# Kernel optimization log

Measured on AMD Instinct MI355X. Metric: run time of the kernel, lower is better.

Reference implementation:

```python
import jax, jax.numpy as jnp
import numpy as np

N_NODES = 50000
N_EDGES = 640000
HIDDEN = 128
EDGE_DIM = 3


def _glorot(key, shape):
    fan_in, fan_out = shape[0], shape[1]
    lim = (6.0 / (fan_in + fan_out)) ** 0.5
    return jax.random.uniform(key, shape, jnp.float32, -lim, lim)


def setup_inputs() -> dict:
    key = jax.random.key(0)
    ks = jax.random.split(key, 12)
    x = jax.random.normal(ks[0], (N_NODES, HIDDEN), jnp.float32)
    edge_index = jax.random.randint(ks[1], (2, N_EDGES), 0, N_NODES, jnp.int64)
    edge_attr = jax.random.normal(ks[2], (N_EDGES, EDGE_DIM), jnp.float32)
    params = {
        "W_msg1": _glorot(ks[3], (2 * HIDDEN + EDGE_DIM, HIDDEN)),
        "b_msg1": jnp.zeros((HIDDEN,), jnp.float32),
        "W_msg2": _glorot(ks[4], (HIDDEN, HIDDEN)),
        "b_msg2": jnp.zeros((HIDDEN,), jnp.float32),
        "W_gate": _glorot(ks[5], (2 * HIDDEN, HIDDEN)),
        "b_gate": jnp.zeros((HIDDEN,), jnp.float32),
        "W_upd1": _glorot(ks[6], (2 * HIDDEN, HIDDEN)),
        "b_upd1": jnp.zeros((HIDDEN,), jnp.float32),
        "W_upd2": _glorot(ks[7], (HIDDEN, HIDDEN)),
        "b_upd2": jnp.zeros((HIDDEN,), jnp.float32),
        "ln_gamma": jnp.ones((HIDDEN,), jnp.float32),
        "ln_beta": jnp.zeros((HIDDEN,), jnp.float32),
    }
    return dict(x=x, edge_index=edge_index, edge_attr=edge_attr, **params)


def reference(x, edge_index, edge_attr, W_msg1, b_msg1, W_msg2, b_msg2,
              W_gate, b_gate, W_upd1, b_upd1, W_upd2, b_upd2, ln_gamma, ln_beta):
    src, dst = edge_index[0], edge_index[1]
    source = x[src]            # [E, H]
    target = x[dst]            # [E, H]
    msg_in = jnp.concatenate([source, target, edge_attr], axis=-1)  # [E, 2H+edge_dim]
    h = jax.nn.relu(msg_in @ W_msg1 + b_msg1)  # dropout is identity in eval
    messages = h @ W_msg2 + b_msg2             # [E, H]
    aggregated = jax.ops.segment_sum(messages, dst, num_segments=x.shape[0])  # [N, H]
    upd_in = jnp.concatenate([x, aggregated], axis=-1)  # [N, 2H]
    gate = jax.nn.sigmoid(upd_in @ W_gate + b_gate)
    update = jax.nn.relu(upd_in @ W_upd1 + b_upd1) @ W_upd2 + b_upd2
    out = gate * update + (1.0 - gate) * x
    # LayerNorm (eps=1e-5, matching torch default)
    mu = jnp.mean(out, axis=-1, keepdims=True)
    var = jnp.var(out, axis=-1, keepdims=True)
    normed = (out - mu) * jax.lax.rsqrt(var + 1e-5)
    return normed * ln_gamma + ln_beta
```

## Files before the change

kernel.cpp:

```cpp
#include <hip/hip_runtime.h>
#include <hip/hip_bf16.h>

#define HID 128

typedef __attribute__((ext_vector_type(8))) short short8;
typedef __attribute__((ext_vector_type(4))) float f32x4;

__device__ __forceinline__ unsigned short f2bf(float f) {
    unsigned int u = __builtin_bit_cast(unsigned int, f);
    u += 0x7FFFu + ((u >> 16) & 1u);
    return (unsigned short)(u >> 16);
}
__device__ __forceinline__ float bf2f(unsigned short h) {
    unsigned int u = ((unsigned int)h) << 16;
    return __builtin_bit_cast(float, u);
}

__global__ void prep_w(const float* __restrict__ W, unsigned short* __restrict__ Wf, int nks) {
    int t = blockIdx.x * 256 + threadIdx.x;
    if (t >= nks * 8 * 64) return;
    int lane = t & 63, nt = (t >> 6) & 7, ks = t >> 9;
    int kb  = ks * 32 + ((lane >> 4) << 3);
    int col = (nt << 4) + (lane & 15);
    union { unsigned short u[8]; uint4 q; } p;
    #pragma unroll
    for (int j = 0; j < 8; ++j) p.u[j] = f2bf(W[(size_t)(kb + j) * 128 + col]);
    *(uint4*)(Wf + (size_t)t * 8) = p.q;
}

__global__ void prep_comp(const float* __restrict__ Wtop,
                          const float* __restrict__ Wm2,
                          const float* __restrict__ b2,
                          unsigned short* __restrict__ Wh,
                          float* __restrict__ bc)
{
    int t = blockIdx.x * 256 + threadIdx.x;
    if (t < 32768) {
        int j = t & 7, lane = (t >> 3) & 63, nt = (t >> 9) & 7, ks = t >> 12;
        int r   = ks * 32 + ((lane >> 4) << 3) + j;
        int col = (nt << 4) + (lane & 15);
        float w;
        if (r < 128) {
            w = Wtop[(size_t)r * 128 + col];
        } else {
            const float* a = Wm2 + (size_t)(r - 128) * 128;
            float s = 0.f;
            for (int k = 0; k < 128; ++k)
                s = fmaf(a[k], Wtop[(size_t)(128 + k) * 128 + col], s);
            w = s;
        }
        Wh[t] = f2bf(w);
    }
    if (blockIdx.x == 0 && threadIdx.x < 128) {
        int jj = threadIdx.x;
        float s = 0.f;
        for (int k = 0; k < 128; ++k)
            s = fmaf(b2[k], Wtop[(size_t)(128 + k) * 128 + jj], s);
        bc[jj] = s;
    }
}

__global__ void hist_k(const int* __restrict__ ei, unsigned* __restrict__ cnt, int E) {
    int e = blockIdx.x * 256 + threadIdx.x;
    if (e < E) atomicAdd(&cnt[ei[E + e]], 1u);
}

__global__ void scan_k(const unsigned* __restrict__ cnt, unsigned* __restrict__ cur, int n) {
    __shared__ unsigned wsum[16];
    int tid = threadIdx.x, lane = tid & 63, w = tid >> 6;
    unsigned carry = 0;
    for (int base = 0; base < n; base += 4096) {
        int i = base + tid * 4;
        unsigned v0 = 0, v1 = 0, v2 = 0, v3 = 0;
        if (i + 3 < n) {
            uint4 q = *(const uint4*)(cnt + i);
            v0 = q.x; v1 = q.y; v2 = q.z; v3 = q.w;
        } else {
            if (i < n)     v0 = cnt[i];
            if (i + 1 < n) v1 = cnt[i + 1];
            if (i + 2 < n) v2 = cnt[i + 2];
            if (i + 3 < n) v3 = cnt[i + 3];
        }
        unsigned t0 = v0, t1 = t0 + v1, t2 = t1 + v2, t3 = t2 + v3;
        unsigned s = t3;
        #pragma unroll
        for (int off = 1; off < 64; off <<= 1) {
            unsigned t = __shfl_up(s, off);
            if (lane >= off) s += t;
        }
        if (lane == 63) wsum[w] = s;
        __syncthreads();
        if (tid < 16) {
            unsigned t = wsum[tid];
            #pragma unroll
            for (int off = 1; off < 16; off <<= 1) {
                unsigned u = __shfl_up(t, off);
                if (tid >= off) t += u;
            }
            wsum[tid] = t;
        }
        __syncthreads();
        unsigned woff = (w == 0) ? 0u : wsum[w - 1];
        unsigned excl = carry + woff + (s - t3);
        if (i < n)     cur[i]     = excl;
        if (i + 1 < n) cur[i + 1] = excl + t0;
        if (i + 2 < n) cur[i + 2] = excl + t1;
        if (i + 3 < n) cur[i + 3] = excl + t2;
        unsigned tot = wsum[15];
        __syncthreads();
        carry += tot;
    }
}

__global__ void scatter_k(const int* __restrict__ ei, const float* __restrict__ ea,
                          unsigned* __restrict__ cur, uint4* __restrict__ rec, int E) {
    int e = blockIdx.x * 256 + threadIdx.x;
    if (e >= E) return;
    int d = ei[E + e];
    unsigned pos = atomicAdd(&cur[d], 1u);
    uint4 r;
    r.x = (unsigned)ei[e];
    r.y = __builtin_bit_cast(unsigned, ea[(size_t)e * 3 + 0]);
    r.z = __builtin_bit_cast(unsigned, ea[(size_t)e * 3 + 1]);
    r.w = __builtin_bit_cast(unsigned, ea[(size_t)e * 3 + 2]);
    rec[pos] = r;
}

__global__ __launch_bounds__(256, 2)
void s1t_gemm(const float* __restrict__ x, const unsigned short* __restrict__ W1f,
              unsigned short* __restrict__ S1b, unsigned short* __restrict__ Tb, int N)
{
    __shared__ alignas(16) unsigned short sW[32768];
    const int tid  = threadIdx.x;
    for (int i = tid; i < 4096; i += 256)
        ((uint4*)sW)[i] = ((const uint4*)W1f)[i];
    __syncthreads();

    const int lane = tid & 63;
    const int wid  = tid >> 6;
    const int n0   = (blockIdx.x * 4 + wid) * 16;
    if (n0 >= N) return;
    const int arow = lane & 15;
    const int g4   = lane >> 4;

    int nr = n0 + arow; if (nr >= N) nr = N - 1;
    const float* px = x + (size_t)nr * 128 + g4 * 8;

    short8 af[4];
    #pragma unroll
    for (int ks = 0; ks < 4; ++ks) {
        float4 v0 = *(const float4*)(px + ks * 32);
        float4 v1 = *(const float4*)(px + ks * 32 + 4);
        float v[8] = { v0.x, v0.y, v0.z, v0.w, v1.x, v1.y, v1.z, v1.w };
        #pragma unroll
        for (int j = 0; j < 8; ++j) af[ks][j] = (short)f2bf(v[j]);
    }

    f32x4 s1[8], tt[8];
    #pragma unroll
    for (int i = 0; i < 8; ++i) { s1[i] = (f32x4)0.f; tt[i] = (f32x4)0.f; }
    #pragma unroll
    for (int ks = 0; ks < 4; ++ks) {
        #pragma unroll
        for (int nt = 0; nt < 8; ++nt) {
            short8 b1 = *(const short8*)(sW + (size_t)((ks * 8 + nt) * 64 + lane) * 8);
            short8 b2 = *(const short8*)(sW + (size_t)(((ks + 4) * 8 + nt) * 64 + lane) * 8);
            s1[nt] = __builtin_amdgcn_mfma_f32_16x16x32_bf16(af[ks], b1, s1[nt], 0, 0, 0);
            tt[nt] = __builtin_amdgcn_mfma_f32_16x16x32_bf16(af[ks], b2, tt[nt], 0, 0, 0);
        }
    }
    #pragma unroll
    for (int nt = 0; nt < 8; ++nt) {
        int col = nt * 16 + arow;
        #pragma unroll
        for (int r = 0; r < 4; ++r) {
            int node = n0 + g4 * 4 + r;
            if (node < N) {
                S1b[(size_t)node * 128 + col] = f2bf(s1[nt][r]);
                Tb [(size_t)node * 128 + col] = f2bf(tt[nt][r]);
            }
        }
    }
}

__global__ __launch_bounds__(256, 8)
void csr_edge_k(const unsigned short* __restrict__ S1b, const unsigned short* __restrict__ Tb,
                const uint4* __restrict__ rec,
                const unsigned* __restrict__ cnt, const unsigned* __restrict__ cur,
                const float* __restrict__ W1tail, const float* __restrict__ bm1,
                float* __restrict__ HS, int N)
{
    const int lane = threadIdx.x & 63;
    const int wid  = threadIdx.x >> 6;
    const int gw   = blockIdx.x * 4 + wid;
    const int stride = gridDim.x * 4;
    const int c2 = lane * 2;

    const float w00 = W1tail[c2],       w01 = W1tail[c2 + 1];
    const float w10 = W1tail[128 + c2], w11 = W1tail[128 + c2 + 1];
    const float w20 = W1tail[256 + c2], w21 = W1tail[256 + c2 + 1];
    const float b0  = bm1[c2],          b1v = bm1[c2 + 1];

    for (int d = gw; d < N; d += stride) {
        int e1 = (int)cur[d];
        int c  = (int)cnt[d];
        int e0 = e1 - c;
        unsigned tv = *(const unsigned*)(Tb + (size_t)d * 128 + c2);
        float t0 = bf2f((unsigned short)(tv & 0xffff)) + b0;
        float t1 = bf2f((unsigned short)(tv >> 16))    + b1v;
        float a0 = 0.f, a1 = 0.f;
        if (c > 0) {
            uint4 r0 = rec[e0];
            uint4 r1 = (c > 1) ? rec[e0 + 1] : make_uint4(0u, 0u, 0u, 0u);
            unsigned sv0 = *(const unsigned*)(S1b + (size_t)r0.x * 128 + c2);
            for (int e = e0; e < e1; ++e) {
                uint4 r2 = (e + 2 < e1) ? rec[e + 2] : make_uint4(0u, 0u, 0u, 0u);
                unsigned sv1 = (e + 1 < e1)
                    ? *(const unsigned*)(S1b + (size_t)r1.x * 128 + c2) : 0u;
                float x0 = __builtin_bit_cast(float, r0.y);
                float x1 = __builtin_bit_cast(float, r0.z);
                float x2 = __builtin_bit_cast(float, r0.w);
                float h0 = bf2f((unsigned short)(sv0 & 0xffff)) + t0;
                float h1 = bf2f((unsigned short)(sv0 >> 16))    + t1;
                h0 = fmaf(x0, w00, h0); h0 = fmaf(x1, w10, h0); h0 = fmaf(x2, w20, h0);
                h1 = fmaf(x0, w01, h1); h1 = fmaf(x1, w11, h1); h1 = fmaf(x2, w21, h1);
                a0 += fmaxf(h0, 0.f);
                a1 += fmaxf(h1, 0.f);
                r0 = r1; r1 = r2; sv0 = sv1;
            }
        }
        float2 o; o.x = a0; o.y = a1;
        *(float2*)(HS + (size_t)d * 128 + c2) = o;
    }
}

__global__ __launch_bounds__(256, 8)
void atomic_edge_k(const unsigned short* __restrict__ S1b, const unsigned short* __restrict__ Tb,
                   const int* __restrict__ ei, const float* __restrict__ ea,
                   const float* __restrict__ W1tail, const float* __restrict__ bm1,
                   float* __restrict__ HS, int E)
{
    const int lane = threadIdx.x & 63;
    const int wid  = threadIdx.x >> 6;
    const int gw   = blockIdx.x * 4 + wid;
    const int stride = gridDim.x * 4;
    const int c2 = lane * 2;

    const float w00 = W1tail[c2],       w01 = W1tail[c2 + 1];
    const float w10 = W1tail[128 + c2], w11 = W1tail[128 + c2 + 1];
    const float w20 = W1tail[256 + c2], w21 = W1tail[256 + c2 + 1];
    const float b0  = bm1[c2],          b1v = bm1[c2 + 1];

    for (int e = gw; e < E; e += stride) {
        int s = ei[e], d = ei[E + e];
        float x0 = ea[(size_t)e * 3 + 0];
        float x1 = ea[(size_t)e * 3 + 1];
        float x2 = ea[(size_t)e * 3 + 2];
        unsigned tv = *(const unsigned*)(Tb + (size_t)d * 128 + c2);
        unsigned sv = *(const unsigned*)(S1b + (size_t)s * 128 + c2);
        float h0 = bf2f((unsigned short)(sv & 0xffff)) + bf2f((unsigned short)(tv & 0xffff)) + b0;
        float h1 = bf2f((unsigned short)(sv >> 16))    + bf2f((unsigned short)(tv >> 16))    + b1v;
        h0 = fmaf(x0, w00, h0); h0 = fmaf(x1, w10, h0); h0 = fmaf(x2, w20, h0);
        h1 = fmaf(x0, w01, h1); h1 = fmaf(x1, w11, h1); h1 = fmaf(x2, w21, h1);
        unsafeAtomicAdd(HS + (size_t)d * 128 + c2,     fmaxf(h0, 0.f));
        unsafeAtomicAdd(HS + (size_t)d * 128 + c2 + 1, fmaxf(h1, 0.f));
    }
}

__global__ __launch_bounds__(256, 2)
void node_mfma(const float* __restrict__ x,
               const float* __restrict__ HS,
               const unsigned* __restrict__ cnt,
               const float* __restrict__ bcg, const float* __restrict__ bcu,
               const unsigned short* __restrict__ WgH,
               const unsigned short* __restrict__ Wu1H,
               const unsigned short* __restrict__ Wu2H,
               const float* __restrict__ bg, const float* __restrict__ bu1,
               const float* __restrict__ bu2,
               const float* __restrict__ gamma, const float* __restrict__ beta,
               float* __restrict__ out, int N)
{
    __shared__ alignas(16) char smem[49152];

    const int tid  = threadIdx.x;
    const int lane = tid & 63;
    const int wid  = tid >> 6;
    const int n0   = (blockIdx.x * 4 + wid) * 16;

    const int arow = lane & 15;
    const int g4   = lane >> 4;

    int nr = n0 + arow; if (nr >= N) nr = N - 1;
    if (nr < 0) nr = 0;
    const float* px = x  + (size_t)nr * 128 + g4 * 8;
    const float* pa = HS + (size_t)nr * 128 + g4 * 8;

    short8 ah[8], al[8];
    #pragma unroll
    for (int ks = 0; ks < 8; ++ks) {
        const float* p = (ks < 4) ? (px + ks * 32) : (pa + (ks - 4) * 32);
        float4 v0 = *(const float4*)p;
        float4 v1 = *(const float4*)(p + 4);
        float v[8] = { v0.x, v0.y, v0.z, v0.w, v1.x, v1.y, v1.z, v1.w };
        #pragma unroll
        for (int j = 0; j < 8; ++j) {
            unsigned short h = f2bf(v[j]);
            ah[ks][j] = (short)h;
            al[ks][j] = (short)f2bf(v[j] - bf2f(h));
        }
    }

    float degf[4];
    #pragma unroll
    for (int r = 0; r < 4; ++r) {
        int node = n0 + g4 * 4 + r;
        degf[r] = (node >= 0 && node < N) ? (float)cnt[node] : 0.f;
    }

    f32x4 ga[8], ua[8];
    #pragma unroll
    for (int i = 0; i < 8; ++i) { ga[i] = (f32x4)0.f; ua[i] = (f32x4)0.f; }

    uint4* sB4 = (uint4*)smem;
    const unsigned short* sB = (const unsigned short*)smem;
    for (int ks = 0; ks < 8; ++ks) {
        #pragma unroll
        for (int i = 0; i < 2; ++i) {
            int idx = tid + i * 256;
            sB4[idx]       = ((const uint4*)WgH )[ks * 512 + idx];
            sB4[512 + idx] = ((const uint4*)Wu1H)[ks * 512 + idx];
        }
        __syncthreads();
        #pragma unroll
        for (int nt = 0; nt < 8; ++nt) {
            size_t o = (size_t)(nt * 64 + lane) * 8;
            short8 bh = *(const short8*)(sB + o);
            short8 uh = *(const short8*)(sB + 4096 + o);
            ga[nt] = __builtin_amdgcn_mfma_f32_16x16x32_bf16(ah[ks], bh, ga[nt], 0, 0, 0);
            ga[nt] = __builtin_amdgcn_mfma_f32_16x16x32_bf16(al[ks], bh, ga[nt], 0, 0, 0);
            ua[nt] = __builtin_amdgcn_mfma_f32_16x16x32_bf16(ah[ks], uh, ua[nt], 0, 0, 0);
            ua[nt] = __builtin_amdgcn_mfma_f32_16x16x32_bf16(al[ks], uh, ua[nt], 0, 0, 0);
        }
        __syncthreads();
    }

    #pragma unroll
    for (int nt = 0; nt < 8; ++nt) {
        int col = nt * 16 + arow;
        float bgc = bcg[col], buc = bcu[col];
        #pragma unroll
        for (int r = 0; r < 4; ++r) {
            ga[nt][r] = fmaf(degf[r], bgc, ga[nt][r]);
            ua[nt][r] = fmaf(degf[r], buc, ua[nt][r]);
        }
    }

    char* Hw = smem + 16384 + wid * 8192;
    #pragma unroll
    for (int nt = 0; nt < 8; ++nt) {
        int col = nt * 16 + arow;
        float b1 = bu1[col];
        #pragma unroll
        for (int r = 0; r < 4; ++r) {
            int row = g4 * 4 + r;
            float u = fmaxf(ua[nt][r] + b1, 0.f);
            unsigned short h = f2bf(u);
            unsigned short l = f2bf(u - bf2f(h));
            unsigned int pk = (unsigned int)h | ((unsigned int)l << 16);
            *(unsigned int*)(Hw + row * 512 + ((col * 4) ^ ((row & 15) << 4))) = pk;
        }
    }

    #pragma unroll
    for (int nt = 0; nt < 8; ++nt) {
        int col = nt * 16 + arow;
        float b = bg[col];
        #pragma unroll
        for (int r = 0; r < 4; ++r)
            ga[nt][r] = 1.f / (1.f + expf(-(ga[nt][r] + b)));
    }
    __syncthreads();

    f32x4 u2[8];
    #pragma unroll
    for (int i = 0; i < 8; ++i) u2[i] = (f32x4)0.f;
    for (int ks = 0; ks < 4; ++ks) {
        {
            int idx = tid;
            sB4[idx] = ((const uint4*)Wu2H)[ks * 512 + idx];
            sB4[256 + idx] = ((const uint4*)Wu2H)[ks * 512 + 256 + idx];
        }
        __syncthreads();
        int b0 = ks * 128 + g4 * 32;
        unsigned int q0[4], q1[4];
        *(uint4*)q0 = *(const uint4*)(Hw + arow * 512 + ( b0       ^ (arow << 4)));
        *(uint4*)q1 = *(const uint4*)(Hw + arow * 512 + ((b0 + 16) ^ (arow << 4)));
        short8 a2h, a2l;
        #pragma unroll
        for (int j = 0; j < 4; ++j) {
            a2h[j]     = (short)(q0[j] & 0xffff);
            a2l[j]     = (short)(q0[j] >> 16);
            a2h[4 + j] = (short)(q1[j] & 0xffff);
            a2l[4 + j] = (short)(q1[j] >> 16);
        }
        #pragma unroll
        for (int nt = 0; nt < 8; ++nt) {
            size_t o = (size_t)(nt * 64 + lane) * 8;
            short8 bh = *(const short8*)(sB + o);
            u2[nt] = __builtin_amdgcn_mfma_f32_16x16x32_bf16(a2h, bh, u2[nt], 0, 0, 0);
            u2[nt] = __builtin_amdgcn_mfma_f32_16x16x32_bf16(a2l, bh, u2[nt], 0, 0, 0);
        }
        __syncthreads();
    }

    float s[4]  = {0.f, 0.f, 0.f, 0.f};
    float ss[4] = {0.f, 0.f, 0.f, 0.f};
    #pragma unroll
    for (int nt = 0; nt < 8; ++nt) {
        int col = nt * 16 + arow;
        float b2 = bu2[col];
        #pragma unroll
        for (int r = 0; r < 4; ++r) {
            int node = n0 + g4 * 4 + r;
            int nc = (node >= 0 && node < N) ? node : 0;
            float xv = x[(size_t)nc * 128 + col];
            float g  = ga[nt][r];
            float o  = g * (u2[nt][r] + b2) + (1.f - g) * xv;
            u2[nt][r] = o;
            s[r]  += o;
            ss[r] += o * o;
        }
    }
    #pragma unroll
    for (int off = 8; off >= 1; off >>= 1) {
        #pragma unroll
        for (int r = 0; r < 4; ++r) {
            s[r]  += __shfl_xor(s[r],  off);
            ss[r] += __shfl_xor(ss[r], off);
        }
    }
    float mu[4], rstd[4];
    #pragma unroll
    for (int r = 0; r < 4; ++r) {
        mu[r] = s[r] * (1.f / 128.f);
        float var = ss[r] * (1.f / 128.f) - mu[r] * mu[r];
        rstd[r] = rsqrtf(var + 1e-5f);
    }
    #pragma unroll
    for (int nt = 0; nt < 8; ++nt) {
        int col = nt * 16 + arow;
        float gm = gamma[col], bt = beta[col];
        #pragma unroll
        for (int r = 0; r < 4; ++r) {
            int node = n0 + g4 * 4 + r;
            if (node >= 0 && node < N)
                out[(size_t)node * 128 + col] = (u2[nt][r] - mu[r]) * rstd[r] * gm + bt;
        }
    }
}

extern "C" void kernel_launch(void* const* d_in, const int* in_sizes, int n_in,
                              void* d_out, int out_size, void* d_ws, size_t ws_size,
                              hipStream_t stream)
{
    const float* x    = (const float*)d_in[0];
    const int*   ei   = (const int*)  d_in[1];
    const float* ea   = (const float*)d_in[2];
    const float* Wm1  = (const float*)d_in[3];
    const float* bm1  = (const float*)d_in[4];
    const float* Wm2  = (const float*)d_in[5];
    const float* bm2  = (const float*)d_in[6];
    const float* Wg   = (const float*)d_in[7];
    const float* bg   = (const float*)d_in[8];
    const float* Wu1  = (const float*)d_in[9];
    const float* bu1  = (const float*)d_in[10];
    const float* Wu2  = (const float*)d_in[11];
    const float* bu2  = (const float*)d_in[12];
    const float* gmma = (const float*)d_in[13];
    const float* beta = (const float*)d_in[14];
    float* out = (float*)d_out;

    const int N = in_sizes[0] / HID;
    const int E = in_sizes[1] / 2;

    unsigned short* S1b  = (unsigned short*)d_ws;
    unsigned short* Tb   = S1b + (size_t)N * HID;
    float*          HS   = (float*)(Tb + (size_t)N * HID);
    unsigned short* W1f  = (unsigned short*)(HS + (size_t)N * HID);
    unsigned short* WgH  = W1f + 32768;
    unsigned short* Wu1H = WgH + 32768;
    unsigned short* Wu2H = Wu1H + 32768;
    float*          bcg  = (float*)(Wu2H + 16384);
    float*          bcu  = bcg + 128;
    unsigned*       cnt  = (unsigned*)(bcu + 128);
    unsigned*       cur  = cnt + N;
    uint4*          rec  = (uint4*)(cur + N);
    rec = (uint4*)(((size_t)rec + 15) & ~(size_t)15);
    size_t need_sort = (size_t)((char*)(rec + E) - (char*)d_ws);
    const bool tierA = (ws_size >= need_sort);

    prep_w<<<dim3(16), dim3(256), 0, stream>>>(Wm1, W1f, 8);
    prep_comp<<<dim3(128), dim3(256), 0, stream>>>(Wg,  Wm2, bm2, WgH,  bcg);
    prep_comp<<<dim3(128), dim3(256), 0, stream>>>(Wu1, Wm2, bm2, Wu1H, bcu);
    prep_w<<<dim3(8), dim3(256), 0, stream>>>(Wu2, Wu2H, 4);

    s1t_gemm<<<dim3((N + 63) / 64), dim3(256), 0, stream>>>(x, W1f, S1b, Tb, N);

    hipMemsetAsync(cnt, 0, (size_t)N * sizeof(unsigned), stream);
    hist_k<<<dim3((E + 255) / 256), dim3(256), 0, stream>>>(ei, cnt, E);

    if (tierA) {
        scan_k<<<dim3(1), dim3(1024), 0, stream>>>(cnt, cur, N);
        scatter_k<<<dim3((E + 255) / 256), dim3(256), 0, stream>>>(ei, ea, cur, rec, E);
        csr_edge_k<<<dim3(2048), dim3(256), 0, stream>>>(
            S1b, Tb, rec, cnt, cur, Wm1 + 256 * HID, bm1, HS, N);
    } else {
        hipMemsetAsync(HS, 0, (size_t)N * HID * sizeof(float), stream);
        atomic_edge_k<<<dim3(2048), dim3(256), 0, stream>>>(
            S1b, Tb, ei, ea, Wm1 + 256 * HID, bm1, HS, E);
    }

    node_mfma<<<dim3((N + 63) / 64), dim3(256), 0, stream>>>(
        x, HS, cnt, bcg, bcu,
        WgH, Wu1H, Wu2H,
        bg, bu1, bu2, gmma, beta, out, N);
}
```

Before: 241.4 us.

## Fuse weight-prep kernels with cnt zeroing, deepen edge prefetch, double-buffer node weights

```diff
diff --git a/kernel.cpp b/kernel.cpp
--- a/kernel.cpp
+++ b/kernel.cpp
@@ -16,47 +16,77 @@
     return __builtin_bit_cast(float, u);
 }
 
-__global__ void prep_w(const float* __restrict__ W, unsigned short* __restrict__ Wf, int nks) {
-    int t = blockIdx.x * 256 + threadIdx.x;
-    if (t >= nks * 8 * 64) return;
-    int lane = t & 63, nt = (t >> 6) & 7, ks = t >> 9;
-    int kb  = ks * 32 + ((lane >> 4) << 3);
-    int col = (nt << 4) + (lane & 15);
-    union { unsigned short u[8]; uint4 q; } p;
-    #pragma unroll
-    for (int j = 0; j < 8; ++j) p.u[j] = f2bf(W[(size_t)(kb + j) * 128 + col]);
-    *(uint4*)(Wf + (size_t)t * 8) = p.q;
-}
-
-__global__ void prep_comp(const float* __restrict__ Wtop,
-                          const float* __restrict__ Wm2,
-                          const float* __restrict__ b2,
-                          unsigned short* __restrict__ Wh,
-                          float* __restrict__ bc)
+__global__ void prep_all(const float* __restrict__ Wm1,
+                         const float* __restrict__ Wg,  const float* __restrict__ Wu1,
+                         const float* __restrict__ Wm2, const float* __restrict__ bm2,
+                         const float* __restrict__ Wu2,
+                         unsigned short* __restrict__ W1f,
+                         unsigned short* __restrict__ WgH,  float* __restrict__ bcg,
+                         unsigned short* __restrict__ Wu1H, float* __restrict__ bcu,
+                         unsigned short* __restrict__ Wu2H,
+                         unsigned* __restrict__ cnt, int N)
 {
-    int t = blockIdx.x * 256 + threadIdx.x;
-    if (t < 32768) {
-        int j = t & 7, lane = (t >> 3) & 63, nt = (t >> 9) & 7, ks = t >> 12;
-        int r   = ks * 32 + ((lane >> 4) << 3) + j;
-        int col = (nt << 4) + (lane & 15);
-        float w;
-        if (r < 128) {
-            w = Wtop[(size_t)r * 128 + col];
-        } else {
-            const float* a = Wm2 + (size_t)(r - 128) * 128;
+    int b = blockIdx.x;
+    if (b < 16) {
+        int t = b * 256 + threadIdx.x;
+        if (t < 4096) {
+            int lane = t & 63, nt = (t >> 6) & 7, ks = t >> 9;
+            int kb  = ks * 32 + ((lane >> 4) << 3);
+            int col = (nt << 4) + (lane & 15);
+            union { unsigned short u[8]; uint4 q; } p;
+            #pragma unroll
+            for (int j = 0; j < 8; ++j) p.u[j] = f2bf(Wm1[(size_t)(kb + j) * 128 + col]);
+            *(uint4*)(W1f + (size_t)t * 8) = p.q;
+        }
+    } else if (b < 272) {
+        const bool isG = (b < 144);
+        const float* Wtop = isG ? Wg : Wu1;
+        unsigned short* Wh = isG ? WgH : Wu1H;
+        float* bc = isG ? bcg : bcu;
+        int lb = b - (isG ? 16 : 144);
+        int t = lb * 256 + threadIdx.x;
+        if (t < 32768) {
+            int j = t & 7, lane = (t >> 3) & 63, nt = (t >> 9) & 7, ks = t >> 12;
+            int r   = ks * 32 + ((lane >> 4) << 3) + j;
+            int col = (nt << 4) + (lane & 15);
+            float w;
+            if (r < 128) {
+                w = Wtop[(size_t)r * 128 + col];
+            } else {
+                const float* a = Wm2 + (size_t)(r - 128) * 128;
+                float s = 0.f;
+                for (int k = 0; k < 128; ++k)
+                    s = fmaf(a[k], Wtop[(size_t)(128 + k) * 128 + col], s);
+                w = s;
+            }
+            Wh[t] = f2bf(w);
+        }
+        if (lb == 0 && threadIdx.x < 128) {
+            int jj = threadIdx.x;
             float s = 0.f;
             for (int k = 0; k < 128; ++k)
-                s = fmaf(a[k], Wtop[(size_t)(128 + k) * 128 + col], s);
-            w = s;
-        }
-        Wh[t] = f2bf(w);
-    }
-    if (blockIdx.x == 0 && threadIdx.x < 128) {
-        int jj = threadIdx.x;
-        float s = 0.f;
-        for (int k = 0; k < 128; ++k)
-            s = fmaf(b2[k], Wtop[(size_t)(128 + k) * 128 + jj], s);
-        bc[jj] = s;
+                s = fmaf(bm2[k], Wtop[(size_t)(128 + k) * 128 + jj], s);
+            bc[jj] = s;
+        }
+    } else if (b < 280) {
+        int t = (b - 272) * 256 + threadIdx.x;
+        if (t < 2048) {
+            int lane = t & 63, nt = (t >> 6) & 7, ks = t >> 9;
+            int kb  = ks * 32 + ((lane >> 4) << 3);
+            int col = (nt << 4) + (lane & 15);
+            union { unsigned short u[8]; uint4 q; } p;
+            #pragma unroll
+            for (int j = 0; j < 8; ++j) p.u[j] = f2bf(Wu2[(size_t)(kb + j) * 128 + col]);
+            *(uint4*)(Wu2H + (size_t)t * 8) = p.q;
+        }
+    } else {
+        int t = (b - 280) * 256 + threadIdx.x;
+        int i = t * 4;
+        if (i + 3 < N) {
+            *(uint4*)(cnt + i) = make_uint4(0u, 0u, 0u, 0u);
+        } else {
+            for (int k = 0; k < 4 && i + k < N; ++k) cnt[i + k] = 0u;
+        }
     }
 }
 
@@ -211,22 +241,26 @@
         float a0 = 0.f, a1 = 0.f;
         if (c > 0) {
             uint4 r0 = rec[e0];
-            uint4 r1 = (c > 1) ? rec[e0 + 1] : make_uint4(0u, 0u, 0u, 0u);
-            unsigned sv0 = *(const unsigned*)(S1b + (size_t)r0.x * 128 + c2);
+            uint4 r1 = (e0 + 1 < e1) ? rec[e0 + 1] : r0;
+            uint4 r2 = (e0 + 2 < e1) ? rec[e0 + 2] : r0;
+            uint4 r3 = (e0 + 3 < e1) ? rec[e0 + 3] : r0;
+            unsigned s0 = *(const unsigned*)(S1b + (size_t)r0.x * 128 + c2);
+            unsigned s1 = (e0 + 1 < e1)
+                ? *(const unsigned*)(S1b + (size_t)r1.x * 128 + c2) : 0u;
             for (int e = e0; e < e1; ++e) {
-                uint4 r2 = (e + 2 < e1) ? rec[e + 2] : make_uint4(0u, 0u, 0u, 0u);
-                unsigned sv1 = (e + 1 < e1)
-                    ? *(const unsigned*)(S1b + (size_t)r1.x * 128 + c2) : 0u;
                 float x0 = __builtin_bit_cast(float, r0.y);
                 float x1 = __builtin_bit_cast(float, r0.z);
                 float x2 = __builtin_bit_cast(float, r0.w);
-                float h0 = bf2f((unsigned short)(sv0 & 0xffff)) + t0;
-                float h1 = bf2f((unsigned short)(sv0 >> 16))    + t1;
+                float h0 = bf2f((unsigned short)(s0 & 0xffff)) + t0;
+                float h1 = bf2f((unsigned short)(s0 >> 16))    + t1;
                 h0 = fmaf(x0, w00, h0); h0 = fmaf(x1, w10, h0); h0 = fmaf(x2, w20, h0);
                 h1 = fmaf(x0, w01, h1); h1 = fmaf(x1, w11, h1); h1 = fmaf(x2, w21, h1);
                 a0 += fmaxf(h0, 0.f);
                 a1 += fmaxf(h1, 0.f);
-                r0 = r1; r1 = r2; sv0 = sv1;
+                r0 = r1; r1 = r2; r2 = r3;
+                if (e + 4 < e1) r3 = rec[e + 4];
+                s0 = s1;
+                if (e + 2 < e1) s1 = *(const unsigned*)(S1b + (size_t)r1.x * 128 + c2);
             }
         }
         float2 o; o.x = a0; o.y = a1;
@@ -280,7 +314,7 @@
                const float* __restrict__ gamma, const float* __restrict__ beta,
                float* __restrict__ out, int N)
 {
-    __shared__ alignas(16) char smem[49152];
+    __shared__ alignas(16) char smem[65536];
 
     const int tid  = threadIdx.x;
     const int lane = tid & 63;
@@ -317,20 +351,32 @@
         degf[r] = (node >= 0 && node < N) ? (float)cnt[node] : 0.f;
     }
 
+    uint4* buf0 = (uint4*)smem;
+    uint4* buf1 = (uint4*)(smem + 16384);
+
+    {
+        int idx = tid, idx2 = tid + 256;
+        buf0[idx]        = ((const uint4*)WgH )[idx];
+        buf0[idx2]       = ((const uint4*)WgH )[idx2];
+        buf0[512 + idx]  = ((const uint4*)Wu1H)[idx];
+        buf0[512 + idx2] = ((const uint4*)Wu1H)[idx2];
+    }
+    __syncthreads();
+
     f32x4 ga[8], ua[8];
     #pragma unroll
     for (int i = 0; i < 8; ++i) { ga[i] = (f32x4)0.f; ua[i] = (f32x4)0.f; }
 
-    uint4* sB4 = (uint4*)smem;
-    const unsigned short* sB = (const unsigned short*)smem;
     for (int ks = 0; ks < 8; ++ks) {
-        #pragma unroll
-        for (int i = 0; i < 2; ++i) {
-            int idx = tid + i * 256;
-            sB4[idx]       = ((const uint4*)WgH )[ks * 512 + idx];
-            sB4[512 + idx] = ((const uint4*)Wu1H)[ks * 512 + idx];
-        }
-        __syncthreads();
+        const unsigned short* sB = (const unsigned short*)((ks & 1) ? buf1 : buf0);
+        uint4 tg0, tg1, tu0, tu1;
+        if (ks < 7) {
+            int idx = tid, idx2 = tid + 256;
+            tg0 = ((const uint4*)WgH )[(ks + 1) * 512 + idx];
+            tg1 = ((const uint4*)WgH )[(ks + 1) * 512 + idx2];
+            tu0 = ((const uint4*)Wu1H)[(ks + 1) * 512 + idx];
+            tu1 = ((const uint4*)Wu1H)[(ks + 1) * 512 + idx2];
+        }
         #pragma unroll
         for (int nt = 0; nt < 8; ++nt) {
             size_t o = (size_t)(nt * 64 + lane) * 8;
@@ -341,6 +387,14 @@
             ua[nt] = __builtin_amdgcn_mfma_f32_16x16x32_bf16(ah[ks], uh, ua[nt], 0, 0, 0);
             ua[nt] = __builtin_amdgcn_mfma_f32_16x16x32_bf16(al[ks], uh, ua[nt], 0, 0, 0);
         }
+        if (ks < 7) {
+            uint4* nb = (ks & 1) ? buf0 : buf1;
+            int idx = tid, idx2 = tid + 256;
+            nb[idx]        = tg0;
+            nb[idx2]       = tg1;
+            nb[512 + idx]  = tu0;
+            nb[512 + idx2] = tu1;
+        }
         __syncthreads();
     }
 
@@ -355,7 +409,7 @@
         }
     }
 
-    char* Hw = smem + 16384 + wid * 8192;
+    char* Hw = smem + 32768 + wid * 8192;
     #pragma unroll
     for (int nt = 0; nt < 8; ++nt) {
         int col = nt * 16 + arow;
@@ -379,18 +433,25 @@
         for (int r = 0; r < 4; ++r)
             ga[nt][r] = 1.f / (1.f + expf(-(ga[nt][r] + b)));
     }
+
+    {
+        int idx = tid, idx2 = tid + 256;
+        buf0[idx]  = ((const uint4*)Wu2H)[idx];
+        buf0[idx2] = ((const uint4*)Wu2H)[idx2];
+    }
     __syncthreads();
 
     f32x4 u2[8];
     #pragma unroll
     for (int i = 0; i < 8; ++i) u2[i] = (f32x4)0.f;
     for (int ks = 0; ks < 4; ++ks) {
-        {
-            int idx = tid;
-            sB4[idx] = ((const uint4*)Wu2H)[ks * 512 + idx];
-            sB4[256 + idx] = ((const uint4*)Wu2H)[ks * 512 + 256 + idx];
-        }
-        __syncthreads();
+        const unsigned short* sB = (const unsigned short*)((ks & 1) ? buf1 : buf0);
+        uint4 t0v, t1v;
+        if (ks < 3) {
+            int idx = tid, idx2 = tid + 256;
+            t0v = ((const uint4*)Wu2H)[(ks + 1) * 512 + idx];
+            t1v = ((const uint4*)Wu2H)[(ks + 1) * 512 + idx2];
+        }
         int b0 = ks * 128 + g4 * 32;
         unsigned int q0[4], q1[4];
         *(uint4*)q0 = *(const uint4*)(Hw + arow * 512 + ( b0       ^ (arow << 4)));
@@ -409,6 +470,12 @@
             short8 bh = *(const short8*)(sB + o);
             u2[nt] = __builtin_amdgcn_mfma_f32_16x16x32_bf16(a2h, bh, u2[nt], 0, 0, 0);
             u2[nt] = __builtin_amdgcn_mfma_f32_16x16x32_bf16(a2l, bh, u2[nt], 0, 0, 0);
+        }
+        if (ks < 3) {
+            uint4* nb = (ks & 1) ? buf0 : buf1;
+            int idx = tid, idx2 = tid + 256;
+            nb[idx]  = t0v;
+            nb[idx2] = t1v;
         }
         __syncthreads();
     }
@@ -499,14 +566,12 @@
     size_t need_sort = (size_t)((char*)(rec + E) - (char*)d_ws);
     const bool tierA = (ws_size >= need_sort);
 
-    prep_w<<<dim3(16), dim3(256), 0, stream>>>(Wm1, W1f, 8);
-    prep_comp<<<dim3(128), dim3(256), 0, stream>>>(Wg,  Wm2, bm2, WgH,  bcg);
-    prep_comp<<<dim3(128), dim3(256), 0, stream>>>(Wu1, Wm2, bm2, Wu1H, bcu);
-    prep_w<<<dim3(8), dim3(256), 0, stream>>>(Wu2, Wu2H, 4);
+    int zblocks = ((N + 3) / 4 + 255) / 256;
+    prep_all<<<dim3(280 + zblocks), dim3(256), 0, stream>>>(
+        Wm1, Wg, Wu1, Wm2, bm2, Wu2, W1f, WgH, bcg, Wu1H, bcu, Wu2H, cnt, N);
 
     s1t_gemm<<<dim3((N + 63) / 64), dim3(256), 0, stream>>>(x, W1f, S1b, Tb, N);
 
-    hipMemsetAsync(cnt, 0, (size_t)N * sizeof(unsigned), stream);
     hist_k<<<dim3((E + 255) / 256), dim3(256), 0, stream>>>(ei, cnt, E);
 
     if (tierA) {
```

Measured after the change: 228.6 us. 1.06x faster.
